# Kernel tuning notes

Hardware: AMD Instinct MI355X
Metric: run time of the kernel (lower is better)

## Reference

```python
import jax, jax.numpy as jnp
import numpy as np
from jax import lax

T_NO = 200   # filter taps
SUB = 64     # sub_no (C_den.shape[0]); hidden subunits = SUB-1 = 63
E_NO = 2000  # excitatory synapses
I_NO = 500   # inhibitory synapses
T_DATA = 50000
COS_NB = 13
EPS = 1e-8


def make_bases(T_no):
    """Raised-cosine bases exactly as in the torch constructor (numpy constants)."""
    scale, shift = 5.0, 1.0
    x = np.arange(T_no, dtype=np.float64)
    raw = scale * np.log(x + shift + EPS)
    cos_basis = np.zeros((COS_NB, T_no), np.float32)
    for i in range(COS_NB):
        phi = 0.5 * np.pi * i
        b = 0.5 * np.cos(raw - phi) + 0.5
        b[(raw < phi - np.pi) | (raw > phi + np.pi)] = 0.0
        cos_basis[i] = b
    # acausal observation basis: [2*13-1, 2*T_no+1]
    xo = np.arange(-T_no, T_no + 1, dtype=np.float64)
    rawo = scale * np.log(np.abs(xo) + shift + EPS)
    obs_basis = np.zeros((COS_NB * 2 - 1, 2 * T_no + 1), np.float32)
    for i in range(COS_NB):
        phi = 0.5 * np.pi * i
        b = 0.5 * np.cos(rawo - phi) + 0.5
        b[(rawo < phi - np.pi) | (rawo > phi + np.pi)] = 0.0
        if i == 0:
            obs_basis[0] = b
        else:
            obs_basis[2 * i - 1, T_no:] = b[T_no:]      # positive lags
            obs_basis[2 * i, :T_no + 1] = b[:T_no + 1]  # negative lags
    return jnp.asarray(cos_basis), jnp.asarray(obs_basis)


def conv1d(x, kern, groups):
    # x: [1, Cin, L], kern: [Cout, Cin/groups, K] -> [1, Cout, L-K+1]
    return lax.conv_general_dilated(
        x, kern, window_strides=(1,), padding='VALID',
        dimension_numbers=('NCH', 'OIH', 'NCH'), feature_group_count=groups)


def setup_inputs() -> dict:
    key = jax.random.key(0)
    ks = jax.random.split(key, 9)
    return {
        'S_e': jax.random.uniform(ks[0], (T_DATA, E_NO), jnp.float32),
        'S_i': jax.random.uniform(ks[1], (T_DATA, I_NO), jnp.float32),
        'Z_obs': jax.random.normal(ks[2], (T_DATA,), jnp.float32),
        'temp': jnp.float32(0.5),
        'u': jax.random.uniform(ks[3], (T_DATA, SUB - 1, 2), jnp.float32),
        'C_syn_e': jax.random.uniform(ks[4], (SUB, E_NO), jnp.float32),
        'C_syn_i': jax.random.uniform(ks[5], (SUB, I_NO), jnp.float32),
        'W_syn': jax.random.normal(ks[6], (SUB - 1, COS_NB, 2), jnp.float32) * 0.01,
        'W_obs': jax.random.normal(ks[7], (SUB - 1, COS_NB * 2 - 1), jnp.float32) * 0.01,
        'Theta': jax.random.normal(ks[8], (SUB - 1,), jnp.float32) * 0.01,
    }


def reference(S_e, S_i, Z_obs, temp, u, C_syn_e, C_syn_i, W_syn, W_obs, Theta):
    cos_basis, obs_basis = make_bases(T_NO)
    C = W_syn.shape[0]                       # sub_no - 1
    T_data = S_e.shape[0]
    # per-subunit synaptic drive: [T, C]
    syn_e = S_e @ C_syn_e[1:].T
    syn_i = S_i @ C_syn_i[1:].T
    # basis-built causal kernels, flipped as in torch: [C, 1, T_no]
    e_kern = jnp.flip(jnp.einsum('cb,bt->ct', W_syn[:, :, 0], cos_basis), 1)[:, None, :]
    i_kern = jnp.flip(jnp.einsum('cb,bt->ct', W_syn[:, :, 1], cos_basis), 1)[:, None, :]
    # left zero-pad by T_no-1, depthwise grouped conv1d -> [T, C]
    pad_e = jnp.pad(syn_e, ((T_NO - 1, 0), (0, 0))).T[None]  # [1, C, T+T_no-1]
    pad_i = jnp.pad(syn_i, ((T_NO - 1, 0), (0, 0))).T[None]
    filt_e = conv1d(pad_e, e_kern, C)[0].T
    filt_i = conv1d(pad_i, i_kern, C)[0].T
    syn = filt_e + filt_i                    # [T, C]
    # acausal observation filter: 1 -> C channels, kernel 2*T_no+1
    obs_kern = jnp.flip(W_obs @ obs_basis, 1)[:, None, :]    # [C, 1, 2T+1]
    z_pad = jnp.pad(Z_obs, (T_NO, T_NO))[None, None]         # [1, 1, T+2T_no]
    Z_obs_filt = conv1d(z_pad, obs_kern, 1)[0].T             # [T, C]
    # Gumbel-softmax spike sampling over binary logits [L0, 0]
    L0 = syn + Z_obs_filt + Theta                            # [T, C]
    L_hid = jnp.stack([L0, jnp.zeros_like(L0)], axis=2)      # [T, C, 2]
    g = -jnp.log(-jnp.log(u + EPS) + EPS)
    Z_hid = jax.nn.softmax((L_hid + g) / temp, axis=2)[:, :, 0]
    return Z_hid, jax.nn.sigmoid(L0)
```

## Files before the change

### kernel.cpp

```cpp
#include <hip/hip_runtime.h>
#include <math.h>

#define T_NO   200
#define C_NO   63
#define E_NO   2000
#define I_NO   500
#define TD     50000
#define TPAD   50048
#define EPSF   1e-8f

typedef float f32x4 __attribute__((ext_vector_type(4)));
typedef short s16x8 __attribute__((ext_vector_type(8)));

#define WS_HE    0
#define WS_HI    12600
#define WS_HOBS  25200
#define WS_COSB  50464
#define WS_OBSB  53064
#define WS_BE    63104
#define WS_BI    128640
#define WS_PE0   145024
#define PBSZ     3203072
#define WS_PI    9754240
#define WS_L0T   12957312

#define PADW(w) ((w) + (((w) >> 5) << 2))

__device__ inline unsigned short f2bf(float x) {
    unsigned u = __float_as_uint(x);
    return (unsigned short)((u + 0x7FFFu + ((u >> 16) & 1u)) >> 16);
}
__device__ inline unsigned pack2(float lo, float hi) {
    return (unsigned)f2bf(lo) | ((unsigned)f2bf(hi) << 16);
}

__global__ void basis_kernel(float* __restrict__ ws) {
    const double PI = 3.14159265358979323846;
    int idx = blockIdx.x * blockDim.x + threadIdx.x;
    int stride = gridDim.x * blockDim.x;
    for (int p = idx; p < 13 * 200; p += stride) {
        int i = p / 200, t = p - i * 200;
        double raw = 5.0 * log((double)t + 1.0 + 1e-8);
        double phi = 0.5 * PI * (double)i;
        float b = (raw >= phi - PI && raw <= phi + PI) ? (float)(0.5 * cos(raw - phi) + 0.5) : 0.f;
        ws[WS_COSB + p] = b;
    }
    for (int p = idx; p < 25 * 401; p += stride) {
        int j = p / 401, x = p - j * 401;
        int i = (j + 1) >> 1;
        double raw = 5.0 * log(fabs((double)(x - 200)) + 1.0 + 1e-8);
        double phi = 0.5 * PI * (double)i;
        float b = (raw >= phi - PI && raw <= phi + PI) ? (float)(0.5 * cos(raw - phi) + 0.5) : 0.f;
        if (j > 0) {
            if (j & 1) { if (x < 200) b = 0.f; }
            else       { if (x > 200) b = 0.f; }
        }
        ws[WS_OBSB + p] = b;
    }
}

__global__ void prep_kernel(const float* __restrict__ Wsyn, const float* __restrict__ Wobs,
                            const float* __restrict__ Ce, const float* __restrict__ Ci,
                            float* __restrict__ ws) {
    int idx = blockIdx.x * blockDim.x + threadIdx.x;
    int stride = gridDim.x * blockDim.x;
    for (int p = idx; p < 63 * 200; p += stride) {
        int c = p / 200, t = p - c * 200;
        float ae = 0.f, ai = 0.f;
        #pragma unroll
        for (int b = 0; b < 13; ++b) {
            float bv = ws[WS_COSB + b * 200 + t];
            ae += Wsyn[(c * 13 + b) * 2 + 0] * bv;
            ai += Wsyn[(c * 13 + b) * 2 + 1] * bv;
        }
        ws[WS_HE + p] = ae;
        ws[WS_HI + p] = ai;
    }
    for (int p = idx; p < 63 * 401; p += stride) {
        int c = p / 401, x = p - c * 401;
        float a = 0.f;
        #pragma unroll
        for (int j = 0; j < 25; ++j)
            a += Wobs[c * 25 + j] * ws[WS_OBSB + j * 401 + x];
        ws[WS_HOBS + p] = a;
    }
    unsigned short* Be = (unsigned short*)(ws + WS_BE);
    for (int p = idx; p < 64 * 2048; p += stride) {
        int c = p >> 11, k = p & 2047;
        float v = (c < 63 && k < E_NO) ? Ce[(size_t)(c + 1) * E_NO + k] : 0.f;
        Be[p] = f2bf(v);
    }
    unsigned short* Bi = (unsigned short*)(ws + WS_BI);
    for (int p = idx; p < 64 * 512; p += stride) {
        int c = p >> 9, k = p & 511;
        float v = (c < 63 && k < I_NO) ? Ci[(size_t)(c + 1) * I_NO + k] : 0.f;
        Bi[p] = f2bf(v);
    }
}

#define LDA 72
__global__ __launch_bounds__(128, 4) void gemm_kernel(const float* __restrict__ S_e,
                                                      const float* __restrict__ S_i,
                                                      float* __restrict__ ws) {
    __shared__ unsigned int Asu[64 * 36];
    __shared__ unsigned int Bsu[64 * 36];

    const int y = blockIdx.y;
    const bool isE = (y < 3);
    const float* S = isE ? S_e : S_i;
    const unsigned short* Bm = (const unsigned short*)(ws + (isE ? WS_BE : WS_BI));
    const int K     = isE ? E_NO : I_NO;
    const int Kpad  = isE ? 2048 : 512;
    const int kb    = isE ? y * 704 : 0;
    const int nst   = isE ? 11 : 8;
    float* outp = ws + (isE ? (WS_PE0 + (size_t)y * PBSZ) : WS_PI);

    const int tid  = threadIdx.x;
    const int lane = tid & 63;
    const int w    = tid >> 6;
    const int t0   = blockIdx.x * 64;

    const int rA  = tid >> 4;
    const int c4A = tid & 15;
    const int cB  = tid >> 3;
    const int sB  = tid & 7;

    float4 av[8];
    uint4  bv[4];

    auto pf = [&](int s) {
        const int kk = kb + 64 * s;
        const int kA = kk + 4 * c4A;
        #pragma unroll
        for (int g = 0; g < 8; ++g) {
            int t = t0 + rA + 8 * g;
            float4 v = {0.f, 0.f, 0.f, 0.f};
            if (t < TD && kA < K) v = *(const float4*)(S + (size_t)t * K + kA);
            av[g] = v;
        }
        #pragma unroll
        for (int g = 0; g < 4; ++g) {
            int col = cB + 16 * g;
            bv[g] = *(const uint4*)(Bm + (size_t)col * Kpad + kk + sB * 8);
        }
    };

    f32x4 acc[2][4] = {};
    pf(0);
    for (int s = 0; s < nst; ++s) {
        __syncthreads();
        #pragma unroll
        for (int g = 0; g < 8; ++g) {
            int r = rA + 8 * g;
            uint2 w2 = {pack2(av[g].x, av[g].y), pack2(av[g].z, av[g].w)};
            *(uint2*)(Asu + r * 36 + c4A * 2) = w2;
        }
        #pragma unroll
        for (int g = 0; g < 4; ++g) {
            int col = cB + 16 * g;
            *(uint4*)(Bsu + col * 36 + sB * 4) = bv[g];
        }
        __syncthreads();
        if (s + 1 < nst) pf(s + 1);

        const unsigned short* As = (const unsigned short*)Asu;
        const unsigned short* Bs = (const unsigned short*)Bsu;
        const int quad8 = (lane >> 4) * 8;
        #pragma unroll
        for (int ks = 0; ks < 2; ++ks) {
            const int klocal = ks * 32 + quad8;
            s16x8 af[2], bf[4];
            #pragma unroll
            for (int ta = 0; ta < 2; ++ta) {
                int row = 32 * w + 16 * ta + (lane & 15);
                af[ta] = *(const s16x8*)(As + row * LDA + klocal);
            }
            #pragma unroll
            for (int cb = 0; cb < 4; ++cb) {
                int col = 16 * cb + (lane & 15);
                bf[cb] = *(const s16x8*)(Bs + col * LDA + klocal);
            }
            #pragma unroll
            for (int ta = 0; ta < 2; ++ta)
                #pragma unroll
                for (int cb = 0; cb < 4; ++cb)
                    acc[ta][cb] = __builtin_amdgcn_mfma_f32_16x16x32_bf16(af[ta], bf[cb], acc[ta][cb], 0, 0, 0);
        }
    }

    const int cl = lane & 15, rq = 4 * (lane >> 4);
    #pragma unroll
    for (int ta = 0; ta < 2; ++ta)
        #pragma unroll
        for (int cb = 0; cb < 4; ++cb) {
            int c = 16 * cb + cl;
            float* dst = outp + (size_t)c * TPAD + t0 + 32 * w + 16 * ta + rq;
            f32x4 v = acc[ta][cb];
            *(float4*)dst = make_float4(v.x, v.y, v.z, v.w);
        }
}

__device__ inline float4 ldg4(const float* s, int m) {
    return *(const float4*)(s + 4 * m + ((m >> 3) << 2));
}

__global__ __launch_bounds__(256) void fir_kernel(const float* __restrict__ pE0,
                                                  const float* __restrict__ pE1,
                                                  const float* __restrict__ pE2,
                                                  const float* __restrict__ pI0,
                                                  const float* __restrict__ Z,
                                                  const float* __restrict__ he,
                                                  const float* __restrict__ hi,
                                                  const float* __restrict__ ho,
                                                  const float* __restrict__ Theta,
                                                  float* __restrict__ L0T) {
    __shared__ __align__(16) float sE[1392];
    __shared__ __align__(16) float sI[1392];
    __shared__ __align__(16) float zs[1616];
    __shared__ __align__(16) float heS[200];
    __shared__ __align__(16) float hiS[200];
    __shared__ __align__(16) float hoS[404];

    const int c   = blockIdx.y;
    const int t0  = blockIdx.x * 1024;
    const int tid = threadIdx.x;
    const int base = t0 - 203;

    for (int w = tid; w < 1228; w += 256) {
        int t = base + w;
        bool ok = (t >= 0 && t < TD);
        size_t idx = (size_t)c * TPAD + t;
        float ve = 0.f, vi = 0.f;
        if (ok) {
            ve = pE0[idx] + pE1[idx] + pE2[idx];
            vi = pI0[idx];
        }
        sE[PADW(w)] = ve;
        sI[PADW(w)] = vi;
    }
    for (int w = tid; w < 1428; w += 256) {
        int t = base + w;
        zs[PADW(w)] = (t >= 0 && t < TD) ? Z[t] : 0.f;
    }
    for (int d = tid; d < 200; d += 256) { heS[d] = he[c * 200 + d]; hiS[d] = hi[c * 200 + d]; }
    for (int d = tid; d < 401; d += 256) hoS[d] = ho[c * 401 + d];
    __syncthreads();

    const float th = Theta[c];
    float acc[4] = {th, th, th, th};

    {
        float4 eLo = ldg4(sE, tid + 50), eHi = ldg4(sE, tid + 51);
        float4 iLo = ldg4(sI, tid + 50), iHi = ldg4(sI, tid + 51);
        for (int dg = 0; dg < 50; ++dg) {
            const float4 h_e = *(const float4*)(heS + 4 * dg);
            const float4 h_i = *(const float4*)(hiS + 4 * dg);
            const float ew[8] = {eLo.x, eLo.y, eLo.z, eLo.w, eHi.x, eHi.y, eHi.z, eHi.w};
            const float iw[8] = {iLo.x, iLo.y, iLo.z, iLo.w, iHi.x, iHi.y, iHi.z, iHi.w};
            const float heq[4] = {h_e.x, h_e.y, h_e.z, h_e.w};
            const float hiq[4] = {h_i.x, h_i.y, h_i.z, h_i.w};
            #pragma unroll
            for (int q = 0; q < 4; ++q)
                #pragma unroll
                for (int r = 0; r < 4; ++r) {
                    const int o = 3 + r - q;
                    acc[r] += ew[o] * heq[q] + iw[o] * hiq[q];
                }
            eHi = eLo; iHi = iLo;
            if (dg < 49) { eLo = ldg4(sE, tid + 49 - dg); iLo = ldg4(sI, tid + 49 - dg); }
        }
    }
    {
        float4 zLo = ldg4(zs, tid + 100), zHi = ldg4(zs, tid + 101);
        for (int dg = 0; dg < 100; ++dg) {
            const float4 h_o = *(const float4*)(hoS + 4 * dg);
            const float zw[8] = {zLo.x, zLo.y, zLo.z, zLo.w, zHi.x, zHi.y, zHi.z, zHi.w};
            const float hoq[4] = {h_o.x, h_o.y, h_o.z, h_o.w};
            #pragma unroll
            for (int q = 0; q < 4; ++q)
                #pragma unroll
                for (int r = 0; r < 4; ++r) {
                    const int o = 3 + r - q;
                    acc[r] += zw[o] * hoq[q];
                }
            zHi = zLo;
            if (dg < 99) zLo = ldg4(zs, tid + 99 - dg);
        }
        const float h400 = hoS[400];
        #pragma unroll
        for (int r = 0; r < 4; ++r) {
            int w = 4 * tid + 3 + r;
            acc[r] += zs[PADW(w)] * h400;
        }
    }

    const int tb = t0 + 4 * tid;
    if (tb + 3 < TD) {
        float4 v = {acc[0], acc[1], acc[2], acc[3]};
        *(float4*)(L0T + (size_t)c * TPAD + tb) = v;
    } else {
        #pragma unroll
        for (int r = 0; r < 4; ++r)
            if (tb + r < TD) L0T[(size_t)c * TPAD + tb + r] = acc[r];
    }
}

__global__ __launch_bounds__(256) void out_kernel(const float* __restrict__ L0T,
                                                  const float* __restrict__ u,
                                                  const float* __restrict__ temp_p,
                                                  float* __restrict__ out) {
    __shared__ float tile[63 * 65];
    const int t0 = blockIdx.x * 64;
    const int tid = threadIdx.x;

    for (int l = tid; l < 1008; l += 256) {
        int cc = l >> 4;
        int jg = (l & 15) << 2;
        float4 v = *(const float4*)(L0T + (size_t)cc * TPAD + t0 + jg);
        tile[cc * 65 + jg + 0] = v.x;
        tile[cc * 65 + jg + 1] = v.y;
        tile[cc * 65 + jg + 2] = v.z;
        tile[cc * 65 + jg + 3] = v.w;
    }
    __syncthreads();

    const float inv_temp = 1.f / (*temp_p);
    for (int l = tid; l < 4032; l += 256) {
        int tl = l / 63;
        int cc = l - tl * 63;
        int t = t0 + tl;
        if (t < TD) {
            float L0 = tile[cc * 65 + tl];
            float2 uv = *(const float2*)(u + 2 * ((size_t)t * 63 + cc));
            float g0 = -logf(-logf(uv.x + EPSF) + EPSF);
            float g1 = -logf(-logf(uv.y + EPSF) + EPSF);
            float zh = 1.f / (1.f + expf(-((L0 + g0 - g1) * inv_temp)));
            float sg = 1.f / (1.f + expf(-L0));
            out[(size_t)t * 63 + cc] = zh;
            out[3150000 + (size_t)t * 63 + cc] = sg;
        }
    }
}

extern "C" void kernel_launch(void* const* d_in, const int* in_sizes, int n_in,
                              void* d_out, int out_size, void* d_ws, size_t ws_size,
                              hipStream_t stream) {
    (void)in_sizes; (void)n_in; (void)out_size; (void)ws_size;
    const float* S_e   = (const float*)d_in[0];
    const float* S_i   = (const float*)d_in[1];
    const float* Z     = (const float*)d_in[2];
    const float* temp  = (const float*)d_in[3];
    const float* u     = (const float*)d_in[4];
    const float* Ce    = (const float*)d_in[5];
    const float* Ci    = (const float*)d_in[6];
    const float* Wsyn  = (const float*)d_in[7];
    const float* Wobs  = (const float*)d_in[8];
    const float* Theta = (const float*)d_in[9];
    float* out = (float*)d_out;
    float* ws  = (float*)d_ws;

    hipLaunchKernelGGL(basis_kernel, dim3(50), dim3(256), 0, stream, ws);
    hipLaunchKernelGGL(prep_kernel, dim3(256), dim3(256), 0, stream, Wsyn, Wobs, Ce, Ci, ws);
    hipLaunchKernelGGL(gemm_kernel, dim3(782, 4), dim3(128), 0, stream, S_e, S_i, ws);
    hipLaunchKernelGGL(fir_kernel, dim3(49, 63), dim3(256), 0, stream,
                       ws + WS_PE0, ws + WS_PE0 + PBSZ, ws + WS_PE0 + 2 * (size_t)PBSZ,
                       ws + WS_PI, Z,
                       ws + WS_HE, ws + WS_HI, ws + WS_HOBS, Theta, ws + WS_L0T);
    hipLaunchKernelGGL(out_kernel, dim3(782), dim3(256), 0, stream, ws + WS_L0T, u, temp, out);
}
```

Before: 900.3 us.

## Double-buffer GEMM LDS tiles, split E into two K-chunks, stage output via LDS

The GEMM kernel now double-buffers its A/B shared-memory tiles, so each stage needs one barrier instead of two and the next tile's write overlaps with compute. The excitatory K dimension is split into two chunks instead of three, which drops one partial buffer and one read in the FIR kernel. Output accumulators are transposed through LDS so global stores are coalesced along time. In exchange, shared memory doubles and the occupancy hint drops from 4 to 2 blocks, with fewer blocks in flight for the E part.

New measurement: 880.6 us. 1.02x faster.

```diff
diff --git a/kernel.cpp b/kernel.cpp
--- a/kernel.cpp
+++ b/kernel.cpp
@@ -99,20 +99,20 @@
 }
 
 #define LDA 72
-__global__ __launch_bounds__(128, 4) void gemm_kernel(const float* __restrict__ S_e,
+__global__ __launch_bounds__(128, 2) void gemm_kernel(const float* __restrict__ S_e,
                                                       const float* __restrict__ S_i,
                                                       float* __restrict__ ws) {
-    __shared__ unsigned int Asu[64 * 36];
-    __shared__ unsigned int Bsu[64 * 36];
+    __shared__ unsigned int Asu[2][64 * 36];
+    __shared__ unsigned int Bsu[2][64 * 36];
 
     const int y = blockIdx.y;
-    const bool isE = (y < 3);
+    const bool isE = (y < 2);
     const float* S = isE ? S_e : S_i;
     const unsigned short* Bm = (const unsigned short*)(ws + (isE ? WS_BE : WS_BI));
     const int K     = isE ? E_NO : I_NO;
     const int Kpad  = isE ? 2048 : 512;
-    const int kb    = isE ? y * 704 : 0;
-    const int nst   = isE ? 11 : 8;
+    const int kb    = isE ? y * 1024 : 0;
+    const int nst   = isE ? 16 : 8;
     float* outp = ws + (isE ? (WS_PE0 + (size_t)y * PBSZ) : WS_PI);
 
     const int tid  = threadIdx.x;
@@ -145,26 +145,25 @@
         }
     };
 
-    f32x4 acc[2][4] = {};
-    pf(0);
-    for (int s = 0; s < nst; ++s) {
-        __syncthreads();
+    auto wr = [&](int b) {
         #pragma unroll
         for (int g = 0; g < 8; ++g) {
             int r = rA + 8 * g;
             uint2 w2 = {pack2(av[g].x, av[g].y), pack2(av[g].z, av[g].w)};
-            *(uint2*)(Asu + r * 36 + c4A * 2) = w2;
+            *(uint2*)(&Asu[b][r * 36 + c4A * 2]) = w2;
         }
         #pragma unroll
         for (int g = 0; g < 4; ++g) {
             int col = cB + 16 * g;
-            *(uint4*)(Bsu + col * 36 + sB * 4) = bv[g];
-        }
-        __syncthreads();
-        if (s + 1 < nst) pf(s + 1);
-
-        const unsigned short* As = (const unsigned short*)Asu;
-        const unsigned short* Bs = (const unsigned short*)Bsu;
+            *(uint4*)(&Bsu[b][col * 36 + sB * 4]) = bv[g];
+        }
+    };
+
+    f32x4 acc[2][4] = {};
+
+    auto cmp = [&](int b) {
+        const unsigned short* As = (const unsigned short*)Asu[b];
+        const unsigned short* Bs = (const unsigned short*)Bsu[b];
         const int quad8 = (lane >> 4) * 8;
         #pragma unroll
         for (int ks = 0; ks < 2; ++ks) {
@@ -186,18 +185,44 @@
                 for (int cb = 0; cb < 4; ++cb)
                     acc[ta][cb] = __builtin_amdgcn_mfma_f32_16x16x32_bf16(af[ta], bf[cb], acc[ta][cb], 0, 0, 0);
         }
-    }
-
+    };
+
+    pf(0);
+    wr(0);
+    pf(1);
+    __syncthreads();
+
+    for (int s = 0; s < nst; ++s) {
+        cmp(s & 1);
+        if (s + 1 < nst) {
+            wr((s + 1) & 1);
+            if (s + 2 < nst) pf(s + 2);
+        }
+        __syncthreads();
+    }
+
+    float* tile = (float*)Asu;
     const int cl = lane & 15, rq = 4 * (lane >> 4);
     #pragma unroll
     for (int ta = 0; ta < 2; ++ta)
         #pragma unroll
         for (int cb = 0; cb < 4; ++cb) {
             int c = 16 * cb + cl;
-            float* dst = outp + (size_t)c * TPAD + t0 + 32 * w + 16 * ta + rq;
+            int r = 32 * w + 16 * ta + rq;
             f32x4 v = acc[ta][cb];
-            *(float4*)dst = make_float4(v.x, v.y, v.z, v.w);
-        }
+            tile[c * 68 + r + 0] = v.x;
+            tile[c * 68 + r + 1] = v.y;
+            tile[c * 68 + r + 2] = v.z;
+            tile[c * 68 + r + 3] = v.w;
+        }
+    __syncthreads();
+    #pragma unroll
+    for (int g = 0; g < 8; ++g) {
+        int idx = g * 128 + tid;
+        int c = idx >> 4, r4 = (idx & 15) << 2;
+        float4 v = *(const float4*)(tile + c * 68 + r4);
+        *(float4*)(outp + (size_t)c * TPAD + t0 + r4) = v;
+    }
 }
 
 __device__ inline float4 ldg4(const float* s, int m) {
@@ -206,7 +231,6 @@
 
 __global__ __launch_bounds__(256) void fir_kernel(const float* __restrict__ pE0,
                                                   const float* __restrict__ pE1,
-                                                  const float* __restrict__ pE2,
                                                   const float* __restrict__ pI0,
                                                   const float* __restrict__ Z,
                                                   const float* __restrict__ he,
@@ -232,7 +256,7 @@
         size_t idx = (size_t)c * TPAD + t;
         float ve = 0.f, vi = 0.f;
         if (ok) {
-            ve = pE0[idx] + pE1[idx] + pE2[idx];
+            ve = pE0[idx] + pE1[idx];
             vi = pI0[idx];
         }
         sE[PADW(w)] = ve;
@@ -361,9 +385,9 @@
 
     hipLaunchKernelGGL(basis_kernel, dim3(50), dim3(256), 0, stream, ws);
     hipLaunchKernelGGL(prep_kernel, dim3(256), dim3(256), 0, stream, Wsyn, Wobs, Ce, Ci, ws);
-    hipLaunchKernelGGL(gemm_kernel, dim3(782, 4), dim3(128), 0, stream, S_e, S_i, ws);
+    hipLaunchKernelGGL(gemm_kernel, dim3(782, 3), dim3(128), 0, stream, S_e, S_i, ws);
     hipLaunchKernelGGL(fir_kernel, dim3(49, 63), dim3(256), 0, stream,
-                       ws + WS_PE0, ws + WS_PE0 + PBSZ, ws + WS_PE0 + 2 * (size_t)PBSZ,
+                       ws + WS_PE0, ws + WS_PE0 + PBSZ,
                        ws + WS_PI, Z,
                        ws + WS_HE, ws + WS_HI, ws + WS_HOBS, Theta, ws + WS_L0T);
     hipLaunchKernelGGL(out_kernel, dim3(782), dim3(256), 0, stream, ws + WS_L0T, u, temp, out);
```
